# Optimization experiments

Measured on AMD Instinct MI355X. Metric: run time of the kernel, lower is better.

The kernel has to match this reference:

```python
import jax, jax.numpy as jnp
import numpy as np

SPARSITY = 0.8
LOCAL_WINDOW = 64


def setup_inputs() -> dict:
    key = jax.random.key(0)
    k1, k2 = jax.random.split(key)
    B, H, S = 2, 8, 2048
    attention_scores = jax.random.normal(k1, (B, H, S, S), dtype=jnp.float32)
    rand_u = jax.random.uniform(k2, (B, H, S, S), dtype=jnp.float32)
    return {"attention_scores": attention_scores, "rand_u": rand_u}


def reference(attention_scores, rand_u):
    B, H, S, _ = attention_scores.shape
    dt = attention_scores.dtype
    half = LOCAL_WINDOW // 2
    k = max(1, int(S * (1.0 - SPARSITY)))

    idx = jnp.arange(S)
    # local window mask: row i covers columns [max(0,i-half), min(S,i+half))
    local = ((idx[None, :] >= idx[:, None] - half) & (idx[None, :] < idx[:, None] + half)).astype(dt)  # (S,S)

    # global mask: topk over head-averaged importance, shared across heads
    importance = attention_scores.mean(axis=1)  # (B,S,S)
    _, top_g = jax.lax.top_k(importance, k)  # (B,S,k)
    gmask = jnp.zeros((B, S, S), dtype=dt).at[
        jnp.arange(B)[:, None, None], jnp.arange(S)[None, :, None], top_g
    ].set(1.0)

    # random sparsification mask
    random_mask = (rand_u < (1.0 - SPARSITY)).astype(dt)

    combined = ((local[None, None, :, :] + gmask[:, None, :, :] + random_mask) > 0).astype(dt)

    # sparsity enforcement: per-row topk of masked scores -> binary mask
    masked = attention_scores * combined
    _, top_f = jax.lax.top_k(masked, k)  # (B,H,S,k)
    final = jnp.zeros((B, H, S, S), dtype=dt).at[
        jnp.arange(B)[:, None, None, None],
        jnp.arange(H)[None, :, None, None],
        jnp.arange(S)[None, None, :, None],
        top_f,
    ].set(1.0)
    return final
```

## Files before the change

### kernel.cpp

```cpp
#include <hip/hip_runtime.h>
#include <cstdint>
#include <cstddef>

#define S_LEN   2048
#define N_HEADS 8
#define N_BATCH 2
#define TOPK    409
#define HALF_WIN 32
#define NT      256
#define PT      8
#define KEY_P0  0x80000000u
#define KEY_N0  0x7FFFFFFFu

__device__ __forceinline__ unsigned mono(float f) {
  unsigned u = __float_as_uint(f);
  return (u & 0x80000000u) ? ~u : (u | 0x80000000u);
}

__device__ __forceinline__ unsigned mbcnt64(unsigned long long m) {
  return __builtin_amdgcn_mbcnt_hi((unsigned)(m >> 32),
         __builtin_amdgcn_mbcnt_lo((unsigned)m, 0u));
}


struct SelScratch {
  unsigned hist[256];
  unsigned sbuf[256];
  unsigned bk[2];
};

__device__ __forceinline__ unsigned block_sum(unsigned c, SelScratch* s) {
  const int t = threadIdx.x;
  s->sbuf[t] = c;
  __syncthreads();
  #pragma unroll
  for (int d = 128; d > 0; d >>= 1) {
    if (t < d) s->sbuf[t] += s->sbuf[t + d];
    __syncthreads();
  }
  unsigned r = s->sbuf[0];
  __syncthreads();
  return r;
}

__device__ void radix_select(const unsigned* keys, int k, unsigned n0, unsigned n1,
                             SelScratch* s, unsigned* T_out, int* kk_out) {
  const int t = threadIdx.x;
  unsigned prefix = 0, done = 0;
  unsigned kk = (unsigned)k;
  #pragma unroll
  for (int shift = 24; shift >= 0; shift -= 8) {
    s->hist[t] = 0;
    __syncthreads();
    if (t == 0 && n0 != 0 && (KEY_P0 & done) == prefix)
      atomicAdd(&s->hist[(KEY_P0 >> shift) & 255u], n0);
    if (t == 1 && n1 != 0 && (KEY_N0 & done) == prefix)
      atomicAdd(&s->hist[(KEY_N0 >> shift) & 255u], n1);
    #pragma unroll
    for (int q = 0; q < PT; ++q) {
      unsigned kj = keys[t + NT * q];
      if (kj != KEY_P0 && kj != KEY_N0 && (kj & done) == prefix)
        atomicAdd(&s->hist[(kj >> shift) & 255u], 1u);
    }
    __syncthreads();
    s->sbuf[t] = s->hist[t];
    __syncthreads();
    for (int d = 1; d < 256; d <<= 1) {
      unsigned a = (t + d < 256) ? s->sbuf[t + d] : 0u;
      __syncthreads();
      s->sbuf[t] += a;
      __syncthreads();
    }
    unsigned suf_ge = s->sbuf[t];
    unsigned suf_gt = (t < 255) ? s->sbuf[t + 1] : 0u;
    if (suf_gt < kk && kk <= suf_ge) {
      s->bk[0] = (unsigned)t;
      s->bk[1] = kk - suf_gt;
    }
    __syncthreads();
    prefix |= s->bk[0] << shift;
    kk = s->bk[1];
    done |= 0xFFu << shift;
    __syncthreads();
  }
  *T_out = prefix;
  *kk_out = (int)kk;
}

__device__ __forceinline__ int stable_rank_base(int c, SelScratch* s) {
  const int t = threadIdx.x;
  s->sbuf[t] = (unsigned)c;
  __syncthreads();
  for (int d = 1; d < 256; d <<= 1) {
    unsigned a = (t >= d) ? s->sbuf[t - d] : 0u;
    __syncthreads();
    s->sbuf[t] += a;
    __syncthreads();
  }
  int base = (t == 0) ? 0 : (int)s->sbuf[t - 1];
  __syncthreads();
  return base;
}

__global__ __launch_bounds__(NT) void k_gmask(const float* __restrict__ scores,
                                              unsigned* __restrict__ gwords) {
  __shared__ __align__(16) unsigned keys[S_LEN];
  __shared__ SelScratch scr;
  __shared__ __align__(4) unsigned char gb[NT];
  const int t = threadIdx.x;
  const int blk = blockIdx.x;
  const int b = blk >> 11;
  const int i = blk & 2047;
  const size_t base = (((size_t)b * N_HEADS) * S_LEN + i) * S_LEN;

  unsigned c0 = 0, c1 = 0;
  #pragma unroll
  for (int s4 = 0; s4 < 2; ++s4) {
    const int j0 = (t + NT * s4) * 4;
    float4 a = *(const float4*)(scores + base + j0);
    #pragma unroll
    for (int h = 1; h < N_HEADS; ++h) {
      float4 x = *(const float4*)(scores + base + (size_t)h * S_LEN * S_LEN + j0);
      a.x += x.x; a.y += x.y; a.z += x.z; a.w += x.w;
    }
    unsigned kqa[4] __attribute__((aligned(16)));
    kqa[0] = mono(a.x); kqa[1] = mono(a.y); kqa[2] = mono(a.z); kqa[3] = mono(a.w);
    #pragma unroll
    for (int q = 0; q < 4; ++q) {
      c0 += (kqa[q] == KEY_P0);
      c1 += (kqa[q] == KEY_N0);
    }
    *(uint4*)(&keys[j0]) = *(uint4*)kqa;
  }
  __syncthreads();

  unsigned ns = block_sum(c0 | (c1 << 16), &scr);
  unsigned T; int kk;
  radix_select(keys, TOPK, ns & 0xFFFFu, ns >> 16, &scr, &T, &kk);

  int c = 0;
  #pragma unroll
  for (int e = 0; e < PT; ++e) c += (keys[t * PT + e] == T);
  int r = stable_rank_base(c, &scr);

  unsigned byte = 0;
  #pragma unroll
  for (int e = 0; e < PT; ++e) {
    unsigned kj = keys[t * PT + e];
    bool sel;
    if (kj > T)       sel = true;
    else if (kj == T) { sel = (r < kk); ++r; }
    else              sel = false;
    byte |= (unsigned)sel << e;
  }
  gb[t] = (unsigned char)byte;
  __syncthreads();
  if (t < 64) gwords[(size_t)blk * 64 + t] = ((const unsigned*)gb)[t];
}


__global__ __launch_bounds__(64) void k_final(const float* __restrict__ scores,
                                              const float* __restrict__ randu,
                                              const unsigned* __restrict__ gwords,
                                              float* __restrict__ out) {
  __shared__ __align__(16) unsigned hist[256];
  __shared__ unsigned gm[64];
  const int l = threadIdx.x;
  const int blk = blockIdx.x;
  const int i = blk & 2047;
  const int b = blk >> 14;
  const size_t base = (size_t)blk * S_LEN;
  const float thr = (float)(1.0 - 0.8);

  gm[l] = gwords[((size_t)(b << 11) + i) * 64 + l];
  __syncthreads();

  unsigned keys[32];
  unsigned c0 = 0, c1 = 0;
  #pragma unroll
  for (int s = 0; s < 8; ++s) {
    const int j0 = 256 * s + 4 * l;
    float4 sc = *(const float4*)(scores + base + j0);
    float4 ru = *(const float4*)(randu + base + j0);
    const unsigned gmw = gm[8 * s + (l >> 3)];
    const float scv[4] = {sc.x, sc.y, sc.z, sc.w};
    const float ruv[4] = {ru.x, ru.y, ru.z, ru.w};
    #pragma unroll
    for (int e = 0; e < 4; ++e) {
      const int j = j0 + e;
      bool loc = (j >= i - HALF_WIN) && (j < i + HALF_WIN);
      bool g   = (gmw >> (4 * (l & 7) + e)) & 1u;
      bool rnd = ruv[e] < thr;
      unsigned u = __float_as_uint(scv[e]);
      unsigned key;
      if (loc || g || rnd) key = (u & 0x80000000u) ? ~u : (u | 0x80000000u);
      else                 key = (u >> 31) ? KEY_N0 : KEY_P0;
      c0 += (key == KEY_P0);
      c1 += (key == KEY_N0);
      keys[4 * s + e] = key;
    }
  }

  unsigned cs = c0 | (c1 << 16);
  #pragma unroll
  for (int d = 1; d < 64; d <<= 1) cs += __shfl_xor(cs, d);
  const unsigned n0 = cs & 0xFFFFu, n1 = cs >> 16;

  unsigned prefix = 0, done = 0, kk = TOPK;
  unsigned T = 0;
  bool resolved = false;
  #pragma unroll
  for (int pass = 0; pass < 4; ++pass) {
    const int shift = 24 - 8 * pass;
    *(uint4*)&hist[l * 4] = make_uint4(0, 0, 0, 0);
    __syncthreads();
    if (l == 0 && n0 != 0 && (KEY_P0 & done) == prefix)
      atomicAdd(&hist[(KEY_P0 >> shift) & 255u], n0);
    if (l == 1 && n1 != 0 && (KEY_N0 & done) == prefix)
      atomicAdd(&hist[(KEY_N0 >> shift) & 255u], n1);
    #pragma unroll
    for (int q = 0; q < 32; ++q) {
      unsigned kj = keys[q];
      if (kj != KEY_P0 && kj != KEY_N0 && (kj & done) == prefix)
        atomicAdd(&hist[(kj >> shift) & 255u], 1u);
    }
    __syncthreads();
    uint4 hv = *(const uint4*)&hist[l * 4];
    unsigned s3 = hv.w;
    unsigned s2 = hv.z + s3;
    unsigned s1 = hv.y + s2;
    unsigned s0 = hv.x + s1;
    unsigned inc = s0;
    #pragma unroll
    for (int d = 1; d < 64; d <<= 1) {
      unsigned o = __shfl_down(inc, d);
      inc += (l + d < 64) ? o : 0u;
    }
    const unsigned tail = inc - s0;
    const unsigned ge[4] = {s0 + tail, s1 + tail, s2 + tail, s3 + tail};
    const unsigned gt[4] = {s1 + tail, s2 + tail, s3 + tail, tail};
    unsigned packed = 0;
    bool found = false;
    #pragma unroll
    for (int q = 0; q < 4; ++q) {
      if (gt[q] < kk && kk <= ge[q]) {
        packed = ((unsigned)(4 * l + q) << 24) | ((ge[q] - gt[q]) << 12) | (kk - gt[q]);
        found = true;
      }
    }
    unsigned long long bal = __ballot(found);
    int srcl = __ffsll((long long)bal) - 1;
    packed = __shfl(packed, srcl);
    const unsigned cnt = (packed >> 12) & 0xFFFu;
    kk = packed & 0xFFFu;
    prefix |= (packed >> 24) << shift;
    done |= 0xFFu << shift;

    const unsigned m0 = ((KEY_P0 & done) == prefix) ? n0 : 0u;
    const unsigned m1 = ((KEY_N0 & done) == prefix) ? n1 : 0u;
    if (cnt == m0 + m1 && (m0 == 0u || m1 == 0u)) {
      T = m0 ? KEY_P0 : KEY_N0;
      resolved = true;
      break;
    }
    if (cnt == 1u) {
      unsigned cand = 0;
      #pragma unroll
      for (int q = 0; q < 32; ++q) {
        unsigned kj = keys[q];
        if (kj != KEY_P0 && kj != KEY_N0 && (kj & done) == prefix) cand = kj;
      }
      #pragma unroll
      for (int d = 1; d < 64; d <<= 1) cand |= __shfl_xor(cand, d);
      T = cand;
      resolved = true;
      break;
    }
  }
  if (!resolved) T = prefix;

  unsigned S_before = 0;
  #pragma unroll
  for (int s = 0; s < 8; ++s) {
    unsigned long long bal[4];
    unsigned mb[4], own[4];
    #pragma unroll
    for (int e = 0; e < 4; ++e) {
      bal[e] = __ballot(keys[4 * s + e] == T);
      mb[e]  = mbcnt64(bal[e]);
      own[e] = (unsigned)((bal[e] >> l) & 1ull);
    }
    const unsigned cross = S_before + mb[0] + mb[1] + mb[2] + mb[3];
    float v[4] __attribute__((aligned(16)));
    unsigned run = 0;
    #pragma unroll
    for (int e = 0; e < 4; ++e) {
      unsigned kj = keys[4 * s + e];
      bool sel = (kj > T) || (kj == T && (cross + run) < kk);
      run += own[e];
      v[e] = sel ? 1.0f : 0.0f;
    }
    *(float4*)(out + base + 256 * s + 4 * l) = *(const float4*)v;
    S_before += (unsigned)(__popcll(bal[0]) + __popcll(bal[1]) +
                           __popcll(bal[2]) + __popcll(bal[3]));
  }
}

extern "C" void kernel_launch(void* const* d_in, const int* in_sizes, int n_in,
                              void* d_out, int out_size, void* d_ws, size_t ws_size,
                              hipStream_t stream) {
  const float* scores = (const float*)d_in[0];
  const float* randu  = (const float*)d_in[1];
  float* out = (float*)d_out;
  unsigned* gwords = (unsigned*)d_ws;
  k_gmask<<<N_BATCH * S_LEN, NT, 0, stream>>>(scores, gwords);
  k_final<<<N_BATCH * N_HEADS * S_LEN, 64, 0, stream>>>(scores, randu, gwords, out);
}
```

Baseline: 227.2 us.

## Pack four rows per block and split radix select by key range

k_final now processes four rows per 256-thread block, one wavefront per row, each with its own private histogram and gmask slice. Block barriers are replaced by wave-local fences. A count of positive keys decides up front whether the threshold lies among positive keys, the masked zero sentinels, or negative keys, so the radix passes only histogram the relevant range and skip the sentinel bookkeeping. The code relies on wave-synchronous LDS behaviour without __syncthreads, which is a correctness risk if the fences do not order LDS accesses across lanes.

```diff
diff --git a/kernel.cpp b/kernel.cpp
--- a/kernel.cpp
+++ b/kernel.cpp
@@ -159,73 +159,26 @@
 }
 
 
-__global__ __launch_bounds__(64) void k_final(const float* __restrict__ scores,
-                                              const float* __restrict__ randu,
-                                              const unsigned* __restrict__ gwords,
-                                              float* __restrict__ out) {
-  __shared__ __align__(16) unsigned hist[256];
-  __shared__ unsigned gm[64];
-  const int l = threadIdx.x;
-  const int blk = blockIdx.x;
-  const int i = blk & 2047;
-  const int b = blk >> 14;
-  const size_t base = (size_t)blk * S_LEN;
-  const float thr = (float)(1.0 - 0.8);
-
-  gm[l] = gwords[((size_t)(b << 11) + i) * 64 + l];
-  __syncthreads();
-
-  unsigned keys[32];
-  unsigned c0 = 0, c1 = 0;
-  #pragma unroll
-  for (int s = 0; s < 8; ++s) {
-    const int j0 = 256 * s + 4 * l;
-    float4 sc = *(const float4*)(scores + base + j0);
-    float4 ru = *(const float4*)(randu + base + j0);
-    const unsigned gmw = gm[8 * s + (l >> 3)];
-    const float scv[4] = {sc.x, sc.y, sc.z, sc.w};
-    const float ruv[4] = {ru.x, ru.y, ru.z, ru.w};
-    #pragma unroll
-    for (int e = 0; e < 4; ++e) {
-      const int j = j0 + e;
-      bool loc = (j >= i - HALF_WIN) && (j < i + HALF_WIN);
-      bool g   = (gmw >> (4 * (l & 7) + e)) & 1u;
-      bool rnd = ruv[e] < thr;
-      unsigned u = __float_as_uint(scv[e]);
-      unsigned key;
-      if (loc || g || rnd) key = (u & 0x80000000u) ? ~u : (u | 0x80000000u);
-      else                 key = (u >> 31) ? KEY_N0 : KEY_P0;
-      c0 += (key == KEY_P0);
-      c1 += (key == KEY_N0);
-      keys[4 * s + e] = key;
-    }
-  }
-
-  unsigned cs = c0 | (c1 << 16);
-  #pragma unroll
-  for (int d = 1; d < 64; d <<= 1) cs += __shfl_xor(cs, d);
-  const unsigned n0 = cs & 0xFFFFu, n1 = cs >> 16;
-
-  unsigned prefix = 0, done = 0, kk = TOPK;
+__device__ __forceinline__ void radix_range(const unsigned (&keys)[32], unsigned kk0,
+                                            bool pos, unsigned* h, int l,
+                                            unsigned& T_ret, unsigned& kk_ret) {
+  unsigned prefix = 0, done = 0, kk = kk0;
   unsigned T = 0;
   bool resolved = false;
   #pragma unroll
   for (int pass = 0; pass < 4; ++pass) {
     const int shift = 24 - 8 * pass;
-    *(uint4*)&hist[l * 4] = make_uint4(0, 0, 0, 0);
-    __syncthreads();
-    if (l == 0 && n0 != 0 && (KEY_P0 & done) == prefix)
-      atomicAdd(&hist[(KEY_P0 >> shift) & 255u], n0);
-    if (l == 1 && n1 != 0 && (KEY_N0 & done) == prefix)
-      atomicAdd(&hist[(KEY_N0 >> shift) & 255u], n1);
+    *(uint4*)&h[l * 4] = make_uint4(0, 0, 0, 0);
+    __threadfence_block();
     #pragma unroll
     for (int q = 0; q < 32; ++q) {
       unsigned kj = keys[q];
-      if (kj != KEY_P0 && kj != KEY_N0 && (kj & done) == prefix)
-        atomicAdd(&hist[(kj >> shift) & 255u], 1u);
-    }
-    __syncthreads();
-    uint4 hv = *(const uint4*)&hist[l * 4];
+      bool in = pos ? (kj > KEY_P0) : (kj < KEY_N0);
+      if (in && (kj & done) == prefix)
+        atomicAdd(&h[(kj >> shift) & 255u], 1u);
+    }
+    __threadfence_block();
+    uint4 hv = *(const uint4*)&h[l * 4];
     unsigned s3 = hv.w;
     unsigned s2 = hv.z + s3;
     unsigned s1 = hv.y + s2;
@@ -255,20 +208,13 @@
     kk = packed & 0xFFFu;
     prefix |= (packed >> 24) << shift;
     done |= 0xFFu << shift;
-
-    const unsigned m0 = ((KEY_P0 & done) == prefix) ? n0 : 0u;
-    const unsigned m1 = ((KEY_N0 & done) == prefix) ? n1 : 0u;
-    if (cnt == m0 + m1 && (m0 == 0u || m1 == 0u)) {
-      T = m0 ? KEY_P0 : KEY_N0;
-      resolved = true;
-      break;
-    }
     if (cnt == 1u) {
       unsigned cand = 0;
       #pragma unroll
       for (int q = 0; q < 32; ++q) {
         unsigned kj = keys[q];
-        if (kj != KEY_P0 && kj != KEY_N0 && (kj & done) == prefix) cand = kj;
+        bool in = pos ? (kj > KEY_P0) : (kj < KEY_N0);
+        if (in && (kj & done) == prefix) cand = kj;
       }
       #pragma unroll
       for (int d = 1; d < 64; d <<= 1) cand |= __shfl_xor(cand, d);
@@ -278,6 +224,73 @@
     }
   }
   if (!resolved) T = prefix;
+  T_ret = T;
+  kk_ret = kk;
+}
+
+__global__ __launch_bounds__(256) void k_final(const float* __restrict__ scores,
+                                               const float* __restrict__ randu,
+                                               const unsigned* __restrict__ gwords,
+                                               float* __restrict__ out) {
+  __shared__ __align__(16) unsigned hist[4][256];
+  __shared__ unsigned gm[4][64];
+  const int l = threadIdx.x & 63;
+  const int w = threadIdx.x >> 6;
+  const int row = blockIdx.x * 4 + w;
+  const int i = row & 2047;
+  const int b = row >> 14;
+  const size_t base = (size_t)row * S_LEN;
+  const float thr = (float)(1.0 - 0.8);
+  unsigned* h = hist[w];
+  unsigned* g = gm[w];
+
+  g[l] = gwords[((size_t)(b << 11) + i) * 64 + l];
+
+  unsigned keys[32];
+  unsigned c0 = 0, c1 = 0, cp = 0;
+  #pragma unroll
+  for (int s = 0; s < 8; ++s) {
+    const int j0 = 256 * s + 4 * l;
+    float4 sc = *(const float4*)(scores + base + j0);
+    float4 ru = *(const float4*)(randu + base + j0);
+    const unsigned gmw = g[8 * s + (l >> 3)];
+    const float scv[4] = {sc.x, sc.y, sc.z, sc.w};
+    const float ruv[4] = {ru.x, ru.y, ru.z, ru.w};
+    #pragma unroll
+    for (int e = 0; e < 4; ++e) {
+      const int j = j0 + e;
+      bool loc = (j >= i - HALF_WIN) && (j < i + HALF_WIN);
+      bool gbit = (gmw >> (4 * (l & 7) + e)) & 1u;
+      bool rnd = ruv[e] < thr;
+      unsigned u = __float_as_uint(scv[e]);
+      unsigned key;
+      if (loc || gbit || rnd) key = (u & 0x80000000u) ? ~u : (u | 0x80000000u);
+      else                    key = (u >> 31) ? KEY_N0 : KEY_P0;
+      c0 += (key == KEY_P0);
+      c1 += (key == KEY_N0);
+      cp += (key > KEY_P0);
+      keys[4 * s + e] = key;
+    }
+  }
+
+  unsigned cs = c0 | (c1 << 16);
+  #pragma unroll
+  for (int d = 1; d < 64; d <<= 1) {
+    cs += __shfl_xor(cs, d);
+    cp += __shfl_xor(cp, d);
+  }
+  const unsigned n0 = cs & 0xFFFFu, n1 = cs >> 16, np = cp;
+
+  unsigned T, kk;
+  if (TOPK <= np) {
+    radix_range(keys, TOPK, true, h, l, T, kk);
+  } else if (TOPK <= np + n0) {
+    T = KEY_P0; kk = TOPK - np;
+  } else if (TOPK <= np + n0 + n1) {
+    T = KEY_N0; kk = TOPK - np - n0;
+  } else {
+    radix_range(keys, TOPK - np - n0 - n1, false, h, l, T, kk);
+  }
 
   unsigned S_before = 0;
   #pragma unroll
@@ -314,5 +327,5 @@
   float* out = (float*)d_out;
   unsigned* gwords = (unsigned*)d_ws;
   k_gmask<<<N_BATCH * S_LEN, NT, 0, stream>>>(scores, gwords);
-  k_final<<<N_BATCH * N_HEADS * S_LEN, 64, 0, stream>>>(scores, randu, gwords, out);
-}
+  k_final<<<N_BATCH * N_HEADS * S_LEN / 4, 256, 0, stream>>>(scores, randu, gwords, out);
+}
```

Result: slower. 232.9 us (+2.5%).
